# Kernel optimization log

Hardware: AMD Instinct MI355X
Metric: run time of the kernel (lower is better)

## Reference

```python
import jax, jax.numpy as jnp
import numpy as np

N_EMBED = 8192
EMBED_DIM = 4
BETA = 0.25


def setup_inputs() -> dict:
    key = jax.random.key(0)
    k1, k2 = jax.random.split(key)
    z = jax.random.normal(k1, (8, EMBED_DIM, 64, 64), dtype=jnp.float32)
    # torch init: uniform(-1/n_embed, 1/n_embed)
    embed_w = jax.random.uniform(k2, (N_EMBED, EMBED_DIM), dtype=jnp.float32,
                                 minval=-1.0 / N_EMBED, maxval=1.0 / N_EMBED)
    return {"z": z, "embed_w": embed_w}


def reference(z, embed_w):
    # z: [B, C, H, W] -> [B, H, W, C]
    z_nhwc = jnp.transpose(z, (0, 2, 3, 1))
    z_flat = z_nhwc.reshape(-1, EMBED_DIM)  # [N, D]
    # squared L2 distances: ||z||^2 + ||e||^2 - 2 z e^T  -> [N, n_embed]
    d = (jnp.sum(z_flat * z_flat, axis=1, keepdims=True)
         + jnp.sum(embed_w * embed_w, axis=1)
         - 2.0 * z_flat @ embed_w.T)
    min_idx = jnp.argmin(d, axis=1)  # [N] int
    z_q = embed_w[min_idx].reshape(z_nhwc.shape)  # [B, H, W, C]
    sg = jax.lax.stop_gradient
    loss = (jnp.mean((sg(z_q) - z_nhwc) ** 2)
            + BETA * jnp.mean((z_q - sg(z_nhwc)) ** 2))
    # straight-through estimator
    z_q_ste = z_nhwc + sg(z_q - z_nhwc)
    z_q_out = jnp.transpose(z_q_ste, (0, 3, 1, 2))  # back to [B, C, H, W]
    return z_q_out, loss, min_idx
```

## Files before the change

kernel.cpp:

```cpp
#include <hip/hip_runtime.h>
#include <math.h>

typedef float v2f __attribute__((ext_vector_type(2)));

#define N_POINTS 32768
#define NUM_EMBED 8192
#define CH 64
#define CPC (NUM_EMBED / CH)
#define PAIRS (CPC / 2)
#define PPT 8
#define RB 1024
#define RPB (RB / 64)
#define RGRID (N_POINTS / RPB)
#define CSTRIDE 4096

__device__ __forceinline__ v2f pk_mul(v2f a, v2f b) {
    v2f d; asm("v_pk_mul_f32 %0, %1, %2" : "=v"(d) : "v"(a), "v"(b)); return d;
}
__device__ __forceinline__ v2f pk_fma(v2f a, v2f b, v2f c) {
    v2f d; asm("v_pk_fma_f32 %0, %1, %2, %3" : "=v"(d) : "v"(a), "v"(b), "v"(c)); return d;
}

__device__ __forceinline__ unsigned int fkey(float f) {
    unsigned int b = __float_as_uint(f);
    return b ^ (0x80000000u | (unsigned int)((int)b >> 31));
}

__global__ __launch_bounds__(256) void vq_filter_kernel(
        const float* __restrict__ z, const float4* __restrict__ E,
        float* __restrict__ cmax) {
    __shared__ alignas(16) v2f sE[PAIRS * 4];

    const int c = blockIdx.y;
    if (threadIdx.x < CPC) {
        float4 e = E[c * CPC + threadIdx.x];
        int p = threadIdx.x >> 1, h = threadIdx.x & 1;
        float* sf = (float*)sE;
        sf[8 * p + 0 + h] = e.x;
        sf[8 * p + 2 + h] = e.y;
        sf[8 * p + 4 + h] = e.z;
        sf[8 * p + 6 + h] = e.w;
    }

    const int n0 = blockIdx.x * (256 * PPT) + threadIdx.x;

    v2f zv[PPT][4];
    #pragma unroll
    for (int p = 0; p < PPT; ++p) {
        int n = n0 + p * 256;
        int b = n >> 12, hw = n & 4095;
        const float* zp = z + b * 16384 + hw;
        zv[p][0] = (v2f){zp[0], zp[0]};
        zv[p][1] = (v2f){zp[CSTRIDE], zp[CSTRIDE]};
        zv[p][2] = (v2f){zp[2 * CSTRIDE], zp[2 * CSTRIDE]};
        zv[p][3] = (v2f){zp[3 * CSTRIDE], zp[3 * CSTRIDE]};
    }

    __syncthreads();

    float run[PPT];
    #pragma unroll
    for (int p = 0; p < PPT; ++p) run[p] = -__builtin_inff();

    const float4* sE4 = (const float4*)sE;
    #pragma unroll 2
    for (int t = 0; t < PAIRS; ++t) {
        float4 E01 = sE4[2 * t];
        float4 E23 = sE4[2 * t + 1];
        v2f e0 = {E01.x, E01.y};
        v2f e1 = {E01.z, E01.w};
        v2f e2 = {E23.x, E23.y};
        v2f e3 = {E23.z, E23.w};
        #pragma unroll
        for (int p = 0; p < PPT; ++p) {
            v2f dot = pk_mul(zv[p][0], e0);
            dot = pk_fma(zv[p][1], e1, dot);
            dot = pk_fma(zv[p][2], e2, dot);
            dot = pk_fma(zv[p][3], e3, dot);
            run[p] = fmaxf(fmaxf(dot.x, dot.y), run[p]);
        }
    }

    #pragma unroll
    for (int p = 0; p < PPT; ++p)
        cmax[(size_t)c * N_POINTS + n0 + p * 256] = run[p];
}

__global__ __launch_bounds__(RB) void vq_resolve_kernel(
        const float* __restrict__ z, const float4* __restrict__ E,
        const float* __restrict__ cmax,
        float* __restrict__ out, double* __restrict__ partial) {
    __shared__ float sCm[CH][RPB + 1];
    __shared__ double sdata[RPB];
    const int lane = threadIdx.x & 63;
    const int wid = threadIdx.x >> 6;
    const int n0 = blockIdx.x * RPB;
    const int n = n0 + wid;

    {
        int t = threadIdx.x;
        sCm[t >> 4][t & 15] = cmax[(size_t)(t >> 4) * N_POINTS + n0 + (t & 15)];
    }

    const int b = n >> 12;
    const int hw = n & 4095;
    const float* zp = z + b * 16384 + hw;
    float z0 = zp[0];
    float z1 = zp[CSTRIDE];
    float z2 = zp[2 * CSTRIDE];
    float z3 = zp[3 * CSTRIDE];
    float zz = __fmul_rn(z0, z0);
    zz = __fadd_rn(zz, __fmul_rn(z1, z1));
    zz = __fadd_rn(zz, __fmul_rn(z2, z2));
    zz = __fadd_rn(zz, __fmul_rn(z3, z3));

    __syncthreads();

    float cm = sCm[lane][wid];
    float gmax = cm;
    #pragma unroll
    for (int off = 32; off; off >>= 1)
        gmax = fmaxf(gmax, __shfl_xor(gmax, off));

    float u = __fmul_rn(__fadd_rn(zz, 0.01f), 2.38418579e-07f);
    float thr = __fsub_rn(gmax, __fadd_rn(__fadd_rn(u, u), 1e-7f));
    unsigned long long mask = __ballot(cm >= thr);

    unsigned long long bkey = ~0ull;
    while (mask) {
        int c = __builtin_ctzll(mask);
        mask &= mask - 1ull;
        int j0 = c * CPC + lane;
        #pragma unroll
        for (int h = 0; h < 2; ++h) {
            int j = j0 + h * 64;
            float4 e = E[j];
            float ee = __fmul_rn(e.x, e.x);
            ee = __fadd_rn(ee, __fmul_rn(e.y, e.y));
            ee = __fadd_rn(ee, __fmul_rn(e.z, e.z));
            ee = __fadd_rn(ee, __fmul_rn(e.w, e.w));
            float dot = __fmul_rn(z0, e.x);
            dot = __fmaf_rn(z1, e.y, dot);
            dot = __fmaf_rn(z2, e.z, dot);
            dot = __fmaf_rn(z3, e.w, dot);
            float d = __fmaf_rn(-2.0f, dot, __fadd_rn(zz, ee));
            unsigned long long key =
                ((unsigned long long)fkey(d) << 32) | (unsigned int)j;
            bkey = key < bkey ? key : bkey;
        }
    }
    #pragma unroll
    for (int off = 32; off; off >>= 1) {
        unsigned long long o = __shfl_xor(bkey, off);
        bkey = o < bkey ? o : bkey;
    }
    int besti = (int)(unsigned int)(bkey & 0xFFFFFFFFull);

    if (lane == 0) {
        float4 e = E[besti];
        float* op = out + b * 16384 + hw;
        float t0 = __fsub_rn(e.x, z0);
        float t1 = __fsub_rn(e.y, z1);
        float t2 = __fsub_rn(e.z, z2);
        float t3 = __fsub_rn(e.w, z3);
        op[0]           = __fadd_rn(z0, t0);
        op[CSTRIDE]     = __fadd_rn(z1, t1);
        op[2 * CSTRIDE] = __fadd_rn(z2, t2);
        op[3 * CSTRIDE] = __fadd_rn(z3, t3);
        out[131073 + n] = (float)besti;
        double ds = (double)__fmul_rn(t0, t0) + (double)__fmul_rn(t1, t1)
                  + (double)__fmul_rn(t2, t2) + (double)__fmul_rn(t3, t3);
        sdata[wid] = ds;
    }
    __syncthreads();
    if (threadIdx.x == 0) {
        double s = 0.0;
        #pragma unroll
        for (int w = 0; w < RPB; ++w) s += sdata[w];
        partial[blockIdx.x] = s;
    }
}

__global__ void vq_loss_kernel(const double* __restrict__ partial, float* __restrict__ out) {
    __shared__ double sdata[256];
    int t = threadIdx.x;
    double s = 0.0;
    for (int i = t; i < 2048; i += 256) s += partial[i];
    sdata[t] = s;
    __syncthreads();
    #pragma unroll
    for (int st = 128; st > 0; st >>= 1) {
        if (t < st) sdata[t] += sdata[t + st];
        __syncthreads();
    }
    if (t == 0) {
        float m = (float)(sdata[0] / 131072.0);
        out[131072] = __fadd_rn(m, __fmul_rn(0.25f, m));
    }
}

extern "C" void kernel_launch(void* const* d_in, const int* in_sizes, int n_in,
                              void* d_out, int out_size, void* d_ws, size_t ws_size,
                              hipStream_t stream) {
    const float* z = (const float*)d_in[0];
    const float4* E = (const float4*)d_in[1];
    float* out = (float*)d_out;

    char* ws = (char*)d_ws;
    float* cmaxb = (float*)ws;
    double* partial = (double*)(ws + (size_t)CH * N_POINTS * 4);

    vq_filter_kernel<<<dim3(N_POINTS / (256 * PPT), CH), 256, 0, stream>>>(z, E, cmaxb);
    vq_resolve_kernel<<<RGRID, RB, 0, stream>>>(z, E, cmaxb, out, partial);
    vq_loss_kernel<<<1, 256, 0, stream>>>(partial, out);
}
```

Measured before the change: 48.36 us.

## Use fp16 dot2 in the filter pass and batch four points per resolve wave

The coarse filter kernel now packs z and codebook entries into fp16 pairs and uses v_dot2_f32_f16, so each distance takes two dot instructions instead of four packed fp32 ops. The resolve threshold slack is widened with an L1-norm term to cover the extra fp16 rounding error. The resolve kernel shrinks to 256-thread blocks where each wave handles four points serially, and the cmax tile is loaded as float4. The lower filter precision may let more chunks pass the threshold, which adds exact recompute work in the resolve stage, and a slack bound that is too tight could select the wrong index.

```diff
diff --git a/kernel.cpp b/kernel.cpp
--- a/kernel.cpp
+++ b/kernel.cpp
@@ -1,7 +1,8 @@
 #include <hip/hip_runtime.h>
+#include <hip/hip_fp16.h>
 #include <math.h>
 
-typedef float v2f __attribute__((ext_vector_type(2)));
+typedef _Float16 h2 __attribute__((ext_vector_type(2)));
 
 #define N_POINTS 32768
 #define NUM_EMBED 8192
@@ -9,16 +10,28 @@
 #define CPC (NUM_EMBED / CH)
 #define PAIRS (CPC / 2)
 #define PPT 8
-#define RB 1024
-#define RPB (RB / 64)
+#define RB 256
+#define RPB 16
 #define RGRID (N_POINTS / RPB)
 #define CSTRIDE 4096
 
-__device__ __forceinline__ v2f pk_mul(v2f a, v2f b) {
-    v2f d; asm("v_pk_mul_f32 %0, %1, %2" : "=v"(d) : "v"(a), "v"(b)); return d;
-}
-__device__ __forceinline__ v2f pk_fma(v2f a, v2f b, v2f c) {
-    v2f d; asm("v_pk_fma_f32 %0, %1, %2, %3" : "=v"(d) : "v"(a), "v"(b), "v"(c)); return d;
+__device__ __forceinline__ unsigned int pkh(float a, float b) {
+    __half ha = __float2half_rn(a), hb = __float2half_rn(b);
+    unsigned short ua = *reinterpret_cast<unsigned short*>(&ha);
+    unsigned short ub = *reinterpret_cast<unsigned short*>(&hb);
+    return (unsigned int)ua | ((unsigned int)ub << 16);
+}
+
+__device__ __forceinline__ float fdot2(unsigned int a, unsigned int b, float c) {
+#if __has_builtin(__builtin_amdgcn_fdot2)
+    h2 ah = *reinterpret_cast<h2*>(&a);
+    h2 bh = *reinterpret_cast<h2*>(&b);
+    return __builtin_amdgcn_fdot2(ah, bh, c, false);
+#else
+    float d;
+    asm("v_dot2_f32_f16 %0, %1, %2, %3" : "=v"(d) : "v"(a), "v"(b), "v"(c));
+    return d;
+#endif
 }
 
 __device__ __forceinline__ unsigned int fkey(float f) {
@@ -29,31 +42,27 @@
 __global__ __launch_bounds__(256) void vq_filter_kernel(
         const float* __restrict__ z, const float4* __restrict__ E,
         float* __restrict__ cmax) {
-    __shared__ alignas(16) v2f sE[PAIRS * 4];
+    __shared__ alignas(16) uint4 sF[PAIRS];
 
     const int c = blockIdx.y;
     if (threadIdx.x < CPC) {
         float4 e = E[c * CPC + threadIdx.x];
         int p = threadIdx.x >> 1, h = threadIdx.x & 1;
-        float* sf = (float*)sE;
-        sf[8 * p + 0 + h] = e.x;
-        sf[8 * p + 2 + h] = e.y;
-        sf[8 * p + 4 + h] = e.z;
-        sf[8 * p + 6 + h] = e.w;
+        unsigned int* sf = (unsigned int*)sF;
+        sf[4 * p + h]     = pkh(e.x, e.y);
+        sf[4 * p + 2 + h] = pkh(e.z, e.w);
     }
 
     const int n0 = blockIdx.x * (256 * PPT) + threadIdx.x;
 
-    v2f zv[PPT][4];
+    unsigned int z01[PPT], z23[PPT];
     #pragma unroll
     for (int p = 0; p < PPT; ++p) {
         int n = n0 + p * 256;
         int b = n >> 12, hw = n & 4095;
         const float* zp = z + b * 16384 + hw;
-        zv[p][0] = (v2f){zp[0], zp[0]};
-        zv[p][1] = (v2f){zp[CSTRIDE], zp[CSTRIDE]};
-        zv[p][2] = (v2f){zp[2 * CSTRIDE], zp[2 * CSTRIDE]};
-        zv[p][3] = (v2f){zp[3 * CSTRIDE], zp[3 * CSTRIDE]};
+        z01[p] = pkh(zp[0], zp[CSTRIDE]);
+        z23[p] = pkh(zp[2 * CSTRIDE], zp[3 * CSTRIDE]);
     }
 
     __syncthreads();
@@ -62,22 +71,14 @@
     #pragma unroll
     for (int p = 0; p < PPT; ++p) run[p] = -__builtin_inff();
 
-    const float4* sE4 = (const float4*)sE;
-    #pragma unroll 2
+    #pragma unroll 4
     for (int t = 0; t < PAIRS; ++t) {
-        float4 E01 = sE4[2 * t];
-        float4 E23 = sE4[2 * t + 1];
-        v2f e0 = {E01.x, E01.y};
-        v2f e1 = {E01.z, E01.w};
-        v2f e2 = {E23.x, E23.y};
-        v2f e3 = {E23.z, E23.w};
+        uint4 P = sF[t];
         #pragma unroll
         for (int p = 0; p < PPT; ++p) {
-            v2f dot = pk_mul(zv[p][0], e0);
-            dot = pk_fma(zv[p][1], e1, dot);
-            dot = pk_fma(zv[p][2], e2, dot);
-            dot = pk_fma(zv[p][3], e3, dot);
-            run[p] = fmaxf(fmaxf(dot.x, dot.y), run[p]);
+            float dA = fdot2(z01[p], P.x, fdot2(z23[p], P.z, 0.0f));
+            float dB = fdot2(z01[p], P.y, fdot2(z23[p], P.w, 0.0f));
+            run[p] = fmaxf(fmaxf(dA, dB), run[p]);
         }
     }
 
@@ -91,92 +92,100 @@
         const float* __restrict__ cmax,
         float* __restrict__ out, double* __restrict__ partial) {
     __shared__ float sCm[CH][RPB + 1];
-    __shared__ double sdata[RPB];
+    __shared__ double sLoss[RPB];
     const int lane = threadIdx.x & 63;
     const int wid = threadIdx.x >> 6;
     const int n0 = blockIdx.x * RPB;
-    const int n = n0 + wid;
 
     {
         int t = threadIdx.x;
-        sCm[t >> 4][t & 15] = cmax[(size_t)(t >> 4) * N_POINTS + n0 + (t & 15)];
-    }
-
-    const int b = n >> 12;
-    const int hw = n & 4095;
-    const float* zp = z + b * 16384 + hw;
-    float z0 = zp[0];
-    float z1 = zp[CSTRIDE];
-    float z2 = zp[2 * CSTRIDE];
-    float z3 = zp[3 * CSTRIDE];
-    float zz = __fmul_rn(z0, z0);
-    zz = __fadd_rn(zz, __fmul_rn(z1, z1));
-    zz = __fadd_rn(zz, __fmul_rn(z2, z2));
-    zz = __fadd_rn(zz, __fmul_rn(z3, z3));
-
-    __syncthreads();
-
-    float cm = sCm[lane][wid];
-    float gmax = cm;
-    #pragma unroll
-    for (int off = 32; off; off >>= 1)
-        gmax = fmaxf(gmax, __shfl_xor(gmax, off));
-
-    float u = __fmul_rn(__fadd_rn(zz, 0.01f), 2.38418579e-07f);
-    float thr = __fsub_rn(gmax, __fadd_rn(__fadd_rn(u, u), 1e-7f));
-    unsigned long long mask = __ballot(cm >= thr);
-
-    unsigned long long bkey = ~0ull;
-    while (mask) {
-        int c = __builtin_ctzll(mask);
-        mask &= mask - 1ull;
-        int j0 = c * CPC + lane;
-        #pragma unroll
-        for (int h = 0; h < 2; ++h) {
-            int j = j0 + h * 64;
-            float4 e = E[j];
-            float ee = __fmul_rn(e.x, e.x);
-            ee = __fadd_rn(ee, __fmul_rn(e.y, e.y));
-            ee = __fadd_rn(ee, __fmul_rn(e.z, e.z));
-            ee = __fadd_rn(ee, __fmul_rn(e.w, e.w));
-            float dot = __fmul_rn(z0, e.x);
-            dot = __fmaf_rn(z1, e.y, dot);
-            dot = __fmaf_rn(z2, e.z, dot);
-            dot = __fmaf_rn(z3, e.w, dot);
-            float d = __fmaf_rn(-2.0f, dot, __fadd_rn(zz, ee));
-            unsigned long long key =
-                ((unsigned long long)fkey(d) << 32) | (unsigned int)j;
-            bkey = key < bkey ? key : bkey;
-        }
-    }
-    #pragma unroll
-    for (int off = 32; off; off >>= 1) {
-        unsigned long long o = __shfl_xor(bkey, off);
-        bkey = o < bkey ? o : bkey;
-    }
-    int besti = (int)(unsigned int)(bkey & 0xFFFFFFFFull);
-
-    if (lane == 0) {
-        float4 e = E[besti];
-        float* op = out + b * 16384 + hw;
-        float t0 = __fsub_rn(e.x, z0);
-        float t1 = __fsub_rn(e.y, z1);
-        float t2 = __fsub_rn(e.z, z2);
-        float t3 = __fsub_rn(e.w, z3);
-        op[0]           = __fadd_rn(z0, t0);
-        op[CSTRIDE]     = __fadd_rn(z1, t1);
-        op[2 * CSTRIDE] = __fadd_rn(z2, t2);
-        op[3 * CSTRIDE] = __fadd_rn(z3, t3);
-        out[131073 + n] = (float)besti;
-        double ds = (double)__fmul_rn(t0, t0) + (double)__fmul_rn(t1, t1)
-                  + (double)__fmul_rn(t2, t2) + (double)__fmul_rn(t3, t3);
-        sdata[wid] = ds;
+        int row = t >> 2, c4 = (t & 3) * 4;
+        float4 v = *(const float4*)(cmax + (size_t)row * N_POINTS + n0 + c4);
+        sCm[row][c4 + 0] = v.x;
+        sCm[row][c4 + 1] = v.y;
+        sCm[row][c4 + 2] = v.z;
+        sCm[row][c4 + 3] = v.w;
+    }
+    __syncthreads();
+
+    for (int q = 0; q < 4; ++q) {
+        int pl = wid * 4 + q;
+        int n = n0 + pl;
+        int b = n >> 12, hw = n & 4095;
+        const float* zp = z + b * 16384 + hw;
+        float z0 = zp[0];
+        float z1 = zp[CSTRIDE];
+        float z2 = zp[2 * CSTRIDE];
+        float z3 = zp[3 * CSTRIDE];
+        float zz = __fmul_rn(z0, z0);
+        zz = __fadd_rn(zz, __fmul_rn(z1, z1));
+        zz = __fadd_rn(zz, __fmul_rn(z2, z2));
+        zz = __fadd_rn(zz, __fmul_rn(z3, z3));
+
+        float cm = sCm[lane][pl];
+        float gmax = cm;
+        #pragma unroll
+        for (int off = 32; off; off >>= 1)
+            gmax = fmaxf(gmax, __shfl_xor(gmax, off));
+
+        float u = __fmul_rn(__fadd_rn(zz, 0.01f), 2.38418579e-07f);
+        float L1 = __fadd_rn(__fadd_rn(fabsf(z0), fabsf(z1)),
+                             __fadd_rn(fabsf(z2), fabsf(z3)));
+        float slack = __fadd_rn(__fadd_rn(u, u), __fmaf_rn(L1, 4.0e-7f, 3.0e-7f));
+        float thr = __fsub_rn(gmax, slack);
+        unsigned long long mask = __ballot(cm >= thr);
+
+        unsigned long long bkey = ~0ull;
+        while (mask) {
+            int c = __builtin_ctzll(mask);
+            mask &= mask - 1ull;
+            int j0 = c * CPC + lane;
+            #pragma unroll
+            for (int h = 0; h < 2; ++h) {
+                int j = j0 + h * 64;
+                float4 e = E[j];
+                float ee = __fmul_rn(e.x, e.x);
+                ee = __fadd_rn(ee, __fmul_rn(e.y, e.y));
+                ee = __fadd_rn(ee, __fmul_rn(e.z, e.z));
+                ee = __fadd_rn(ee, __fmul_rn(e.w, e.w));
+                float dot = __fmul_rn(z0, e.x);
+                dot = __fmaf_rn(z1, e.y, dot);
+                dot = __fmaf_rn(z2, e.z, dot);
+                dot = __fmaf_rn(z3, e.w, dot);
+                float d = __fmaf_rn(-2.0f, dot, __fadd_rn(zz, ee));
+                unsigned long long key =
+                    ((unsigned long long)fkey(d) << 32) | (unsigned int)j;
+                bkey = key < bkey ? key : bkey;
+            }
+        }
+        #pragma unroll
+        for (int off = 32; off; off >>= 1) {
+            unsigned long long o = __shfl_xor(bkey, off);
+            bkey = o < bkey ? o : bkey;
+        }
+        int besti = (int)(unsigned int)(bkey & 0xFFFFFFFFull);
+
+        if (lane == 0) {
+            float4 e = E[besti];
+            float* op = out + b * 16384 + hw;
+            float t0 = __fsub_rn(e.x, z0);
+            float t1 = __fsub_rn(e.y, z1);
+            float t2 = __fsub_rn(e.z, z2);
+            float t3 = __fsub_rn(e.w, z3);
+            op[0]           = __fadd_rn(z0, t0);
+            op[CSTRIDE]     = __fadd_rn(z1, t1);
+            op[2 * CSTRIDE] = __fadd_rn(z2, t2);
+            op[3 * CSTRIDE] = __fadd_rn(z3, t3);
+            out[131073 + n] = (float)besti;
+            sLoss[pl] = (double)__fmul_rn(t0, t0) + (double)__fmul_rn(t1, t1)
+                      + (double)__fmul_rn(t2, t2) + (double)__fmul_rn(t3, t3);
+        }
     }
     __syncthreads();
     if (threadIdx.x == 0) {
         double s = 0.0;
         #pragma unroll
-        for (int w = 0; w < RPB; ++w) s += sdata[w];
+        for (int w = 0; w < RPB; ++w) s += sLoss[w];
         partial[blockIdx.x] = s;
     }
 }
```

Result: slower. 53.22 us (+10.0%).
